# Optimization experiments

Hardware: AMD Instinct MI355X
Metric: run time of the kernel (lower is better)

The kernel has to match this reference:

```python
import jax, jax.numpy as jnp
import numpy as np

B, N = 4096, 8
C_IMG = 1024          # 256 fpn channels * 4 layers
NODE_CH = 2048        # 8 node concepts * 256
EDGE_CH = 3           # len(edge_concepts) - 1 (HigherPri handled separately)
ACT_CH = 4            # number of unary action predicates
E = N * (N - 1)       # 56 directed edges, fully connected minus self-loops
BBOX_MAX = 1024.0

_idx = np.array([[i, j] for i in range(N) for j in range(N) if i != j], dtype=np.int32)
SRC = jnp.asarray(_idx[:, 0])  # edge_idxs row 0 (message source in PyG NNConv)
DST = jnp.asarray(_idx[:, 1])  # edge_idxs row 1 (aggregation target)


def _lin(key, fin, fout):
    kw, kb = jax.random.split(key)
    s = 1.0 / np.sqrt(fin)
    return (jax.random.uniform(kw, (fin, fout), jnp.float32, -s, s),
            jax.random.uniform(kb, (fout,), jnp.float32, -s, s))


def setup_inputs() -> dict:
    key = jax.random.key(0)
    ks = jax.random.split(key, 16)
    inp = {
        'roi_features': jax.random.normal(ks[0], (B, N, C_IMG), jnp.float32),
        'batch_bboxes': jax.random.uniform(ks[1], (B, N, 4), jnp.float32) * BBOX_MAX,
        'batch_directions': jax.random.normal(ks[2], (B, N, 4), jnp.float32),
        'batch_priorities': jax.random.uniform(ks[3], (B, N), jnp.float32),
    }
    inp['ncp_w1'], inp['ncp_b1'] = _lin(ks[4], C_IMG, 512)
    inp['ncp_w2'], inp['ncp_b2'] = _lin(ks[5], 512, 256)
    inp['ncp_w3'], inp['ncp_b3'] = _lin(ks[6], 256, NODE_CH)
    inp['ep_w1'], inp['ep_b1'] = _lin(ks[7], 8, 256)
    inp['ep_w2'], inp['ep_b2'] = _lin(ks[8], 256, 64)
    inp['ep_w3'], inp['ep_b3'] = _lin(ks[9], 64, (N - 1) * EDGE_CH)
    inp['pr_w1'], inp['pr_b1'] = _lin(ks[10], EDGE_CH + 1, 128)
    inp['pr_w2'], inp['pr_b2'] = _lin(ks[11], 128, NODE_CH * ACT_CH)
    s = 1.0 / np.sqrt(NODE_CH)
    inp['root'] = jax.random.uniform(ks[12], (NODE_CH, ACT_CH), jnp.float32, -s, s)
    inp['bias'] = jnp.zeros((ACT_CH,), jnp.float32)
    return inp


def reference(roi_features, batch_bboxes, batch_directions, batch_priorities,
              ncp_w1, ncp_b1, ncp_w2, ncp_b2, ncp_w3, ncp_b3,
              ep_w1, ep_b1, ep_w2, ep_b2, ep_w3, ep_b3,
              pr_w1, pr_b1, pr_w2, pr_b2, root, bias):
    # node concept predictor: 3-layer MLP + sigmoid over [B, N, C_IMG]
    h = jax.nn.relu(roi_features @ ncp_w1 + ncp_b1)
    h = jax.nn.relu(h @ ncp_w2 + ncp_b2)
    node_concepts = jax.nn.sigmoid(h @ ncp_w3 + ncp_b3)           # [B, N, NODE_CH]

    # edge predictor from bbox (normalized) + direction attributes
    node_attr = jnp.concatenate([batch_bboxes / BBOX_MAX, batch_directions], axis=-1)  # [B,N,8]
    g = jax.nn.relu(node_attr @ ep_w1 + ep_b1)
    g = jax.nn.relu(g @ ep_w2 + ep_b2)
    edge_attr = jax.nn.sigmoid(g @ ep_w3 + ep_b3).reshape(B, N * (N - 1), EDGE_CH)

    # HigherPri channel; original slices pri_mask[:, :, :N-1] (slice [:, :, N:] is empty)
    pri_mask = (batch_priorities[:, :, None] > batch_priorities[:, None, :]).astype(jnp.float32)
    higher_pri = pri_mask[:, :, :N - 1].reshape(B, -1)            # [B, E]
    edge_attr = jnp.concatenate([edge_attr, higher_pri[..., None]], axis=-1)  # [B,E,4]

    # NNConv on batch element 0 only (as in the original forward)
    x = node_concepts[0]                                          # [N, NODE_CH]
    e = edge_attr[0]                                              # [E, EDGE_CH+1]
    w = jax.nn.relu(e @ pr_w1 + pr_b1) @ pr_w2 + pr_b2            # [E, NODE_CH*ACT_CH]
    w = w.reshape(E, NODE_CH, ACT_CH)
    msg = jnp.einsum('ec,eco->eo', x[SRC], w)                     # [E, ACT_CH]
    agg = jax.ops.segment_sum(msg, DST, num_segments=N)           # [N, ACT_CH]
    return agg + x @ root + bias
```

## Files before the change

kernel.cpp:

```cpp
#include <hip/hip_runtime.h>
#include <math.h>

#define CIMG  1024
#define H1F   512
#define H2F   256
#define NODE  2048

#define OFF_H1P  0
#define OFF_X    65536
#define OFF_EW   81920

__global__ __launch_bounds__(256) void k1_l1_edge(
    const float* __restrict__ roi, const float* __restrict__ w1,
    const float* __restrict__ bbox, const float* __restrict__ dir,
    const float* __restrict__ pri,
    const float* __restrict__ ew1, const float* __restrict__ eb1,
    const float* __restrict__ ew2, const float* __restrict__ eb2,
    const float* __restrict__ ew3, const float* __restrict__ eb3,
    const float* __restrict__ pw1, const float* __restrict__ pb1,
    float* __restrict__ h1part, float* __restrict__ ew_out,
    float* __restrict__ out)
{
    __shared__ float smem[2848];
    const int tid = threadIdx.x;
    const int b = blockIdx.x;

    if (b < 32) {
        float* xin = smem;
        const int kbeg = (b >> 1) * 64;
        const int cbase = (b & 1) * 256;
        for (int idx = tid; idx < 512; idx += 256) {
            int r = idx >> 6, kk = idx & 63;
            xin[idx] = roi[r * CIMG + kbeg + kk];
        }
        __syncthreads();
        const int c = cbase + tid;
        float acc[8] = {0, 0, 0, 0, 0, 0, 0, 0};
        const float* Wp = w1 + (size_t)kbeg * H1F + c;
#pragma unroll 4
        for (int kk = 0; kk < 64; ++kk) {
            float w = Wp[(size_t)kk * H1F];
#pragma unroll
            for (int r = 0; r < 8; ++r) acc[r] += xin[r * 64 + kk] * w;
        }
        float* outp = h1part + (b >> 1) * 4096;
#pragma unroll
        for (int r = 0; r < 8; ++r) outp[r * H1F + c] = acc[r];
        return;
    }

    if (tid < 32) out[tid] = 0.f;

    float* attr = smem;
    float* g1   = smem + 64;
    float* g2   = smem + 2112;
    float* ebuf = smem + 2624;

    if (tid < 64) {
        int r = tid >> 3, j = tid & 7;
        attr[r * 8 + j] = (j < 4) ? bbox[r * 4 + j] * (1.0f / 1024.0f)
                                  : dir[r * 4 + (j - 4)];
    }
    __syncthreads();
    {
        int cc = tid;
        for (int r = 0; r < 8; ++r) {
            float s = eb1[cc];
#pragma unroll
            for (int j = 0; j < 8; ++j) s += attr[r * 8 + j] * ew1[j * 256 + cc];
            g1[r * 256 + cc] = s > 0.f ? s : 0.f;
        }
    }
    __syncthreads();
    for (int idx = tid; idx < 512; idx += 256) {
        int r = idx >> 6, cc = idx & 63;
        float s = eb2[cc];
        for (int j = 0; j < 256; ++j) s += g1[r * 256 + j] * ew2[j * 64 + cc];
        g2[idx] = s > 0.f ? s : 0.f;
    }
    __syncthreads();
    if (tid < 168) {
        int r = tid / 21, q = tid % 21;
        float s = eb3[q];
        for (int j = 0; j < 64; ++j) s += g2[r * 64 + j] * ew3[j * 21 + q];
        ebuf[(tid / 3) * 4 + (tid % 3)] = 1.f / (1.f + expf(-s));
    }
    if (tid < 56) {
        ebuf[tid * 4 + 3] = (pri[tid / 7] > pri[tid % 7]) ? 1.f : 0.f;
    }
    __syncthreads();
    for (int idx = tid; idx < 56 * 128; idx += 256) {
        int e = idx >> 7, t = idx & 127;
        float s = pb1[t];
#pragma unroll
        for (int ch = 0; ch < 4; ++ch) s += ebuf[e * 4 + ch] * pw1[ch * 128 + t];
        ew_out[idx] = s > 0.f ? s : 0.f;
    }
}

__global__ __launch_bounds__(1024) void k2_l23(
    const float* __restrict__ h1part, const float* __restrict__ b1,
    const float* __restrict__ w2, const float* __restrict__ b2,
    const float* __restrict__ w3, const float* __restrict__ b3,
    float* __restrict__ x)
{
    __shared__ float h1[4096];
    __shared__ float h2p[8192];
    __shared__ float h2[2048];
    const int tid = threadIdx.x;

    for (int idx = tid; idx < 4096; idx += 1024) {
        int k = idx & 511;
        float v = b1[k];
#pragma unroll
        for (int p = 0; p < 16; ++p) v += h1part[p * 4096 + idx];
        h1[idx] = v > 0.f ? v : 0.f;
    }
    __syncthreads();

    {
        const int c = tid & 255, kg = tid >> 8;
        float acc[8] = {0, 0, 0, 0, 0, 0, 0, 0};
        const float* Wp = w2 + (size_t)(kg * 128) * H2F + c;
        const float* h1p = h1 + kg * 128;
#pragma unroll 4
        for (int kk = 0; kk < 128; ++kk) {
            float w = Wp[(size_t)kk * H2F];
#pragma unroll
            for (int r = 0; r < 8; ++r) acc[r] += h1p[r * 512 + kk] * w;
        }
#pragma unroll
        for (int r = 0; r < 8; ++r) h2p[kg * 2048 + r * 256 + c] = acc[r];
    }
    __syncthreads();
    for (int idx = tid; idx < 2048; idx += 1024) {
        int c = idx & 255;
        float v = b2[c] + h2p[idx] + h2p[2048 + idx] + h2p[4096 + idx] + h2p[6144 + idx];
        h2[idx] = v > 0.f ? v : 0.f;
    }
    __syncthreads();

    {
        const int c = blockIdx.x * 128 + (tid & 127);
        const int r = tid >> 7;
        float acc = b3[c];
        const float* Wp = w3 + c;
        const float* h2r = h2 + r * 256;
#pragma unroll 4
        for (int k = 0; k < 256; ++k)
            acc += h2r[k] * Wp[(size_t)k * NODE];
        x[r * NODE + c] = 1.f / (1.f + expf(-acc));
    }
}

__global__ __launch_bounds__(256) void k3_y2_final(
    const float* __restrict__ x, const float* __restrict__ pw2,
    const float* __restrict__ pb2, const float* __restrict__ root,
    const float* __restrict__ bias, const float* __restrict__ ew,
    float* __restrict__ out)
{
    __shared__ float shx[8192];
    __shared__ float redbuf[128];
    __shared__ float ylocal[32];
    __shared__ float aggl[32];
    __shared__ float dotl[32], xrl[32];
    const int t = blockIdx.x >> 1;
    const int half = blockIdx.x & 1;
    const int tid = threadIdx.x;
    const int lane = tid & 63, wave = tid >> 6;

    if (tid < 32) aggl[tid] = 0.f;
    for (int i = tid; i < 8192; i += 256) {
        int r = i >> 10, cl = i & 1023;
        shx[i] = x[r * NODE + half * 1024 + cl];
    }
    __syncthreads();

    float part[8] = {0, 0, 0, 0, 0, 0, 0, 0};
    const float* row = pw2 + (size_t)t * 8192 + half * 4096;
#pragma unroll 4
    for (int it = 0; it < 16; ++it) {
        int j = tid + it * 256;
        float w = row[j];
        int cl = j >> 2;
#pragma unroll
        for (int s = 0; s < 8; ++s) part[s] += shx[s * 1024 + cl] * w;
    }
#pragma unroll
    for (int s = 0; s < 8; ++s) {
        part[s] += __shfl_xor(part[s], 4);
        part[s] += __shfl_xor(part[s], 8);
        part[s] += __shfl_xor(part[s], 16);
        part[s] += __shfl_xor(part[s], 32);
    }
    if (lane < 4) {
#pragma unroll
        for (int s = 0; s < 8; ++s) redbuf[wave * 32 + s * 4 + lane] = part[s];
    }
    __syncthreads();
    if (tid < 32)
        ylocal[tid] = redbuf[tid] + redbuf[32 + tid] + redbuf[64 + tid] + redbuf[96 + tid];
    __syncthreads();

    if (tid < 224) {
        int e = tid >> 2, o = tid & 3;
        int i = e / 7, jj = e % 7;
        int dst = jj + (jj >= i ? 1 : 0);
        float v = ew[e * 128 + t] * ylocal[i * 4 + o];
        atomicAdd(&aggl[dst * 4 + o], v);
    }
    __syncthreads();
    if (tid < 32) atomicAdd(&out[tid], aggl[tid]);

    if (t == 0) {
#pragma unroll
        for (int si = 0; si < 2; ++si) {
            const int s = wave * 2 + si;
            float pd[4] = {0, 0, 0, 0}, pr[4] = {0, 0, 0, 0};
#pragma unroll 4
            for (int it = 0; it < 16; ++it) {
                int cl = it * 64 + lane;
                float xv = shx[s * 1024 + cl];
                int c = half * 1024 + cl;
                float4 bv = ((const float4*)pb2)[c];
                float4 rv = ((const float4*)root)[c];
                pd[0] += xv * bv.x; pd[1] += xv * bv.y;
                pd[2] += xv * bv.z; pd[3] += xv * bv.w;
                pr[0] += xv * rv.x; pr[1] += xv * rv.y;
                pr[2] += xv * rv.z; pr[3] += xv * rv.w;
            }
#pragma unroll
            for (int o = 0; o < 4; ++o) {
                for (int off = 32; off; off >>= 1) {
                    pd[o] += __shfl_xor(pd[o], off);
                    pr[o] += __shfl_xor(pr[o], off);
                }
            }
            if (lane == 0) {
#pragma unroll
                for (int o = 0; o < 4; ++o) {
                    dotl[s * 4 + o] = pd[o];
                    xrl[s * 4 + o] = pr[o];
                }
            }
        }
        __syncthreads();
        if (tid < 32) {
            int n = tid >> 2, o = tid & 3;
            float totd = 0.f;
#pragma unroll
            for (int s = 0; s < 8; ++s) totd += dotl[s * 4 + o];
            float v = (totd - dotl[n * 4 + o]) + xrl[n * 4 + o]
                    + (half == 0 ? bias[o] : 0.f);
            atomicAdd(&out[tid], v);
        }
    }
}

extern "C" void kernel_launch(void* const* d_in, const int* in_sizes, int n_in,
                              void* d_out, int out_size, void* d_ws, size_t ws_size,
                              hipStream_t stream)
{
    (void)in_sizes; (void)n_in; (void)out_size; (void)ws_size;

    const float* roi    = (const float*)d_in[0];
    const float* bbox   = (const float*)d_in[1];
    const float* dirs   = (const float*)d_in[2];
    const float* pri    = (const float*)d_in[3];
    const float* ncp_w1 = (const float*)d_in[4];
    const float* ncp_b1 = (const float*)d_in[5];
    const float* ncp_w2 = (const float*)d_in[6];
    const float* ncp_b2 = (const float*)d_in[7];
    const float* ncp_w3 = (const float*)d_in[8];
    const float* ncp_b3 = (const float*)d_in[9];
    const float* ep_w1  = (const float*)d_in[10];
    const float* ep_b1  = (const float*)d_in[11];
    const float* ep_w2  = (const float*)d_in[12];
    const float* ep_b2  = (const float*)d_in[13];
    const float* ep_w3  = (const float*)d_in[14];
    const float* ep_b3  = (const float*)d_in[15];
    const float* pr_w1  = (const float*)d_in[16];
    const float* pr_b1  = (const float*)d_in[17];
    const float* pr_w2  = (const float*)d_in[18];
    const float* pr_b2  = (const float*)d_in[19];
    const float* root   = (const float*)d_in[20];
    const float* bias   = (const float*)d_in[21];

    float* ws     = (float*)d_ws;
    float* h1part = ws + OFF_H1P;
    float* x      = ws + OFF_X;
    float* ewbuf  = ws + OFF_EW;
    float* outp   = (float*)d_out;

    k1_l1_edge<<<33, dim3(256), 0, stream>>>(roi, ncp_w1, bbox, dirs, pri,
                                             ep_w1, ep_b1, ep_w2, ep_b2,
                                             ep_w3, ep_b3, pr_w1, pr_b1,
                                             h1part, ewbuf, outp);
    k2_l23<<<16, dim3(1024), 0, stream>>>(h1part, ncp_b1, ncp_w2, ncp_b2,
                                          ncp_w3, ncp_b3, x);
    k3_y2_final<<<256, dim3(256), 0, stream>>>(x, pr_w2, pr_b2, root, bias,
                                               ewbuf, outp);
}
```

Before: 276.3 us.

## Split MLP layers 2 and 3 into separate split-K kernels with partial sums

Replaces the single 16-block fused layer-2/3 kernel, where every block redundantly computed layer 2, with a split-K layer-2 kernel and a split-K layer-3 kernel writing partial sums. The final reduction, bias and sigmoid are folded into the consumer kernel's shared-memory load. Layer 1 gets a finer K split (64 blocks) and float4 shared reads with 4-way unrolled weight loads. The aim is to spread weight streaming over more blocks and remove the redundant work, at the cost of an extra launch and more partial-sum traffic through global memory.

```diff
diff --git a/kernel.cpp b/kernel.cpp
--- a/kernel.cpp
+++ b/kernel.cpp
@@ -7,8 +7,9 @@
 #define NODE  2048
 
 #define OFF_H1P  0
-#define OFF_X    65536
-#define OFF_EW   81920
+#define OFF_H2P  131072
+#define OFF_XP   163840
+#define OFF_EW   229376
 
 __global__ __launch_bounds__(256) void k1_l1_edge(
     const float* __restrict__ roi, const float* __restrict__ w1,
@@ -25,25 +26,32 @@
     const int tid = threadIdx.x;
     const int b = blockIdx.x;
 
-    if (b < 32) {
+    if (b < 64) {
         float* xin = smem;
-        const int kbeg = (b >> 1) * 64;
+        const int kc = b >> 1;
+        const int kbeg = kc * 32;
         const int cbase = (b & 1) * 256;
-        for (int idx = tid; idx < 512; idx += 256) {
-            int r = idx >> 6, kk = idx & 63;
-            xin[idx] = roi[r * CIMG + kbeg + kk];
+        {
+            int r = tid >> 5, kk = tid & 31;
+            xin[tid] = roi[r * CIMG + kbeg + kk];
         }
         __syncthreads();
         const int c = cbase + tid;
         float acc[8] = {0, 0, 0, 0, 0, 0, 0, 0};
         const float* Wp = w1 + (size_t)kbeg * H1F + c;
-#pragma unroll 4
-        for (int kk = 0; kk < 64; ++kk) {
-            float w = Wp[(size_t)kk * H1F];
-#pragma unroll
-            for (int r = 0; r < 8; ++r) acc[r] += xin[r * 64 + kk] * w;
-        }
-        float* outp = h1part + (b >> 1) * 4096;
+#pragma unroll
+        for (int k4 = 0; k4 < 8; ++k4) {
+            float wa = Wp[(size_t)(k4 * 4 + 0) * H1F];
+            float wb = Wp[(size_t)(k4 * 4 + 1) * H1F];
+            float wc = Wp[(size_t)(k4 * 4 + 2) * H1F];
+            float wd = Wp[(size_t)(k4 * 4 + 3) * H1F];
+#pragma unroll
+            for (int r = 0; r < 8; ++r) {
+                float4 xv = *(const float4*)&xin[r * 32 + k4 * 4];
+                acc[r] += xv.x * wa + xv.y * wb + xv.z * wc + xv.w * wd;
+            }
+        }
+        float* outp = h1part + kc * 4096;
 #pragma unroll
         for (int r = 0; r < 8; ++r) outp[r * H1F + c] = acc[r];
         return;
@@ -98,66 +106,89 @@
     }
 }
 
-__global__ __launch_bounds__(1024) void k2_l23(
+__global__ __launch_bounds__(256) void k2_l2(
     const float* __restrict__ h1part, const float* __restrict__ b1,
-    const float* __restrict__ w2, const float* __restrict__ b2,
-    const float* __restrict__ w3, const float* __restrict__ b3,
-    float* __restrict__ x)
-{
-    __shared__ float h1[4096];
-    __shared__ float h2p[8192];
-    __shared__ float h2[2048];
+    const float* __restrict__ w2, float* __restrict__ h2part)
+{
+    __shared__ float xin[256];
     const int tid = threadIdx.x;
-
-    for (int idx = tid; idx < 4096; idx += 1024) {
-        int k = idx & 511;
+    const int kbeg = blockIdx.x * 32;
+
+    {
+        int r = tid >> 5, kk = tid & 31;
+        int k = kbeg + kk;
         float v = b1[k];
 #pragma unroll
-        for (int p = 0; p < 16; ++p) v += h1part[p * 4096 + idx];
-        h1[idx] = v > 0.f ? v : 0.f;
-    }
-    __syncthreads();
-
-    {
-        const int c = tid & 255, kg = tid >> 8;
-        float acc[8] = {0, 0, 0, 0, 0, 0, 0, 0};
-        const float* Wp = w2 + (size_t)(kg * 128) * H2F + c;
-        const float* h1p = h1 + kg * 128;
-#pragma unroll 4
-        for (int kk = 0; kk < 128; ++kk) {
-            float w = Wp[(size_t)kk * H2F];
-#pragma unroll
-            for (int r = 0; r < 8; ++r) acc[r] += h1p[r * 512 + kk] * w;
-        }
-#pragma unroll
-        for (int r = 0; r < 8; ++r) h2p[kg * 2048 + r * 256 + c] = acc[r];
-    }
-    __syncthreads();
-    for (int idx = tid; idx < 2048; idx += 1024) {
-        int c = idx & 255;
-        float v = b2[c] + h2p[idx] + h2p[2048 + idx] + h2p[4096 + idx] + h2p[6144 + idx];
-        h2[idx] = v > 0.f ? v : 0.f;
-    }
-    __syncthreads();
-
-    {
-        const int c = blockIdx.x * 128 + (tid & 127);
-        const int r = tid >> 7;
-        float acc = b3[c];
-        const float* Wp = w3 + c;
-        const float* h2r = h2 + r * 256;
-#pragma unroll 4
-        for (int k = 0; k < 256; ++k)
-            acc += h2r[k] * Wp[(size_t)k * NODE];
-        x[r * NODE + c] = 1.f / (1.f + expf(-acc));
-    }
-}
-
-__global__ __launch_bounds__(256) void k3_y2_final(
-    const float* __restrict__ x, const float* __restrict__ pw2,
-    const float* __restrict__ pb2, const float* __restrict__ root,
-    const float* __restrict__ bias, const float* __restrict__ ew,
-    float* __restrict__ out)
+        for (int p = 0; p < 32; ++p) v += h1part[p * 4096 + r * H1F + k];
+        xin[tid] = v > 0.f ? v : 0.f;
+    }
+    __syncthreads();
+
+    const int c = tid;
+    float acc[8] = {0, 0, 0, 0, 0, 0, 0, 0};
+    const float* Wp = w2 + (size_t)kbeg * H2F + c;
+#pragma unroll
+    for (int k4 = 0; k4 < 8; ++k4) {
+        float wa = Wp[(size_t)(k4 * 4 + 0) * H2F];
+        float wb = Wp[(size_t)(k4 * 4 + 1) * H2F];
+        float wc = Wp[(size_t)(k4 * 4 + 2) * H2F];
+        float wd = Wp[(size_t)(k4 * 4 + 3) * H2F];
+#pragma unroll
+        for (int r = 0; r < 8; ++r) {
+            float4 xv = *(const float4*)&xin[r * 32 + k4 * 4];
+            acc[r] += xv.x * wa + xv.y * wb + xv.z * wc + xv.w * wd;
+        }
+    }
+    float* outp = h2part + blockIdx.x * 2048;
+#pragma unroll
+    for (int r = 0; r < 8; ++r) outp[r * H2F + c] = acc[r];
+}
+
+__global__ __launch_bounds__(256) void k3_l3(
+    const float* __restrict__ h2part, const float* __restrict__ b2,
+    const float* __restrict__ w3, float* __restrict__ xpart)
+{
+    __shared__ float xin[512];
+    const int tid = threadIdx.x;
+    const int kc = blockIdx.x >> 3;
+    const int cbase = (blockIdx.x & 7) * 256;
+    const int kbeg = kc * 64;
+
+    for (int idx = tid; idx < 512; idx += 256) {
+        int r = idx >> 6, kk = idx & 63;
+        int k = kbeg + kk;
+        float v = b2[k];
+#pragma unroll
+        for (int p = 0; p < 16; ++p) v += h2part[p * 2048 + r * H2F + k];
+        xin[idx] = v > 0.f ? v : 0.f;
+    }
+    __syncthreads();
+
+    const int c = cbase + tid;
+    float acc[8] = {0, 0, 0, 0, 0, 0, 0, 0};
+    const float* Wp = w3 + (size_t)kbeg * NODE + c;
+#pragma unroll
+    for (int k4 = 0; k4 < 16; ++k4) {
+        float wa = Wp[(size_t)(k4 * 4 + 0) * NODE];
+        float wb = Wp[(size_t)(k4 * 4 + 1) * NODE];
+        float wc = Wp[(size_t)(k4 * 4 + 2) * NODE];
+        float wd = Wp[(size_t)(k4 * 4 + 3) * NODE];
+#pragma unroll
+        for (int r = 0; r < 8; ++r) {
+            float4 xv = *(const float4*)&xin[r * 64 + k4 * 4];
+            acc[r] += xv.x * wa + xv.y * wb + xv.z * wc + xv.w * wd;
+        }
+    }
+    float* outp = xpart + kc * 16384;
+#pragma unroll
+    for (int r = 0; r < 8; ++r) outp[r * NODE + c] = acc[r];
+}
+
+__global__ __launch_bounds__(256) void k4_y2_final(
+    const float* __restrict__ xpart, const float* __restrict__ b3,
+    const float* __restrict__ pw2, const float* __restrict__ pb2,
+    const float* __restrict__ root, const float* __restrict__ bias,
+    const float* __restrict__ ew, float* __restrict__ out)
 {
     __shared__ float shx[8192];
     __shared__ float redbuf[128];
@@ -172,7 +203,11 @@
     if (tid < 32) aggl[tid] = 0.f;
     for (int i = tid; i < 8192; i += 256) {
         int r = i >> 10, cl = i & 1023;
-        shx[i] = x[r * NODE + half * 1024 + cl];
+        int c = half * 1024 + cl;
+        float v = b3[c];
+#pragma unroll
+        for (int p = 0; p < 4; ++p) v += xpart[p * 16384 + r * NODE + c];
+        shx[i] = 1.f / (1.f + expf(-v));
     }
     __syncthreads();
 
@@ -288,16 +323,17 @@
 
     float* ws     = (float*)d_ws;
     float* h1part = ws + OFF_H1P;
-    float* x      = ws + OFF_X;
+    float* h2part = ws + OFF_H2P;
+    float* xpart  = ws + OFF_XP;
     float* ewbuf  = ws + OFF_EW;
     float* outp   = (float*)d_out;
 
-    k1_l1_edge<<<33, dim3(256), 0, stream>>>(roi, ncp_w1, bbox, dirs, pri,
+    k1_l1_edge<<<65, dim3(256), 0, stream>>>(roi, ncp_w1, bbox, dirs, pri,
                                              ep_w1, ep_b1, ep_w2, ep_b2,
                                              ep_w3, ep_b3, pr_w1, pr_b1,
                                              h1part, ewbuf, outp);
-    k2_l23<<<16, dim3(1024), 0, stream>>>(h1part, ncp_b1, ncp_w2, ncp_b2,
-                                          ncp_w3, ncp_b3, x);
-    k3_y2_final<<<256, dim3(256), 0, stream>>>(x, pr_w2, pr_b2, root, bias,
-                                               ewbuf, outp);
-}
+    k2_l2<<<16, dim3(256), 0, stream>>>(h1part, ncp_b1, ncp_w2, h2part);
+    k3_l3<<<32, dim3(256), 0, stream>>>(h2part, ncp_b2, ncp_w3, xpart);
+    k4_y2_final<<<256, dim3(256), 0, stream>>>(xpart, ncp_b3, pr_w2, pr_b2,
+                                               root, bias, ewbuf, outp);
+}
```

New measurement: 246.9 us. -10.6%, faster.
